# Performance work log

Measured on AMD Instinct MI355X. Metric: run time of the kernel, lower is better.

## Reference

```python
import jax, jax.numpy as jnp
import numpy as np
from jax import lax

E = 300   # word embedding dim (hard-coded embedding_size in DMCNN)
P = 5     # position-feature dim
H = 200   # conv out channels
S = 256   # max_seq_len
L = 34    # num_labels
VOCAB = 21128


def setup_inputs() -> dict:
    key = jax.random.key(0)
    ks = jax.random.split(key, 7)
    B = 8
    return {
        "inputs": jax.random.randint(ks[0], (B, S), 0, VOCAB, dtype=jnp.int64),
        "word_emb": jax.random.normal(ks[1], (VOCAB, E), dtype=jnp.float32) * 0.02,
        "pf_emb": jax.random.normal(ks[2], (S, P), dtype=jnp.float32) * 0.02,
        "conv_W": jax.random.normal(ks[3], (H, E + P, 3), dtype=jnp.float32) * 0.02,
        "conv_b": jax.random.normal(ks[4], (H,), dtype=jnp.float32) * 0.02,
        "fc_W": jax.random.normal(ks[5], (L, 3 * E + 2 * H), dtype=jnp.float32) * 0.02,
        "fc_b": jax.random.normal(ks[6], (L,), dtype=jnp.float32) * 0.02,
    }


def _conv1d(x_ncs, w_oik):
    # x: [N, C, S], w: [O, I, K], stride 1, padding 1 (kernel 3)
    return lax.conv_general_dilated(
        x_ncs, w_oik, window_strides=(1,), padding=[(1, 1)],
        dimension_numbers=("NCH", "OIH", "NCH"))


def reference(inputs, word_emb, pf_emb, conv_W, conv_b, fc_W, fc_b):
    B = inputs.shape[0]
    tok = word_emb[inputs]                       # [B, S, E]

    # Positions i = 1 .. S-2 (the original loop), fully vectorized.
    i_vals = jnp.arange(1, S - 1)                # [S-2]
    j = jnp.arange(S)
    pos_idx = jnp.abs(j[None, :] - i_vals[:, None])   # [S-2, S] == the loop's pos_index
    pf = pf_emb[pos_idx]                         # [S-2, S, P]

    # Conv is linear: split into token part (shared across i) + pf part (per i).
    W_tok, W_pf = conv_W[:, :E, :], conv_W[:, E:, :]
    conv_tok = _conv1d(tok.transpose(0, 2, 1), W_tok) + conv_b[None, :, None]  # [B, H, S]
    conv_pf = _conv1d(pf.transpose(0, 2, 1), W_pf)                             # [S-2, H, S] (batch-independent)

    out = jax.nn.relu(conv_tok[None] + conv_pf[:, None])   # [S-2, B, H, S]

    # Dynamic split max-pool at index i.
    left_mask = (j[None, :] < i_vals[:, None])[:, None, None, :]  # [S-2,1,1,S]
    neg_inf = jnp.array(-jnp.inf, dtype=out.dtype)
    max_left = jnp.where(left_mask, out, neg_inf).max(axis=-1)    # [S-2, B, H]
    max_right = jnp.where(left_mask, neg_inf, out).max(axis=-1)   # [S-2, B, H]
    pool = jnp.concatenate([max_left, max_right], axis=-1)        # [S-2, B, 2H]

    # Lexical-level features: window [i-1, i, i+1] flattened.
    llf = jnp.concatenate([tok[:, 0:S - 2], tok[:, 1:S - 1], tok[:, 2:S]], axis=-1)  # [B, S-2, 3E]

    feat = jnp.concatenate([pool.transpose(1, 0, 2), llf], axis=-1)  # [B, S-2, 2H+3E]
    logits_mid = jnp.einsum("bsf,lf->bsl", feat, fc_W) + fc_b        # [B, S-2, L]

    pad = jnp.zeros((B, 1, L), dtype=logits_mid.dtype).at[:, :, -1].set(1.0)
    return jnp.concatenate([pad, logits_mid, pad], axis=1)          # [B, S, L]
```

## Files before the change

kernel.cpp:

```cpp
#include <hip/hip_runtime.h>

#define E 300
#define P 5
#define H 200
#define S 256
#define L 34
#define B 8
#define NI 254

typedef __attribute__((ext_vector_type(8))) _Float16 half8;
typedef __attribute__((ext_vector_type(2))) _Float16 h2;
typedef __attribute__((ext_vector_type(4))) float f32x4;

#define TOKB_OFF   0
#define TOKB_FL    309632
#define WR3_OFF    309632
#define WR3_FL     96512
#define FCWB_OFF   406144
#define FCWB_FL    32256
#define G_OFF      438400
#define G_FL       51200
#define C0_OFF     489600
#define C0_FL      25400
#define C255_OFF   515000
#define C255_FL    25400
#define CT_OFF     540400
#define CT_FL      204800
#define POOLF_OFF  745200
#define POOLF_FL   425984

__device__ __forceinline__ unsigned short f2h(float f) {
    _Float16 h = (_Float16)f;
    unsigned short u; __builtin_memcpy(&u, &h, 2);
    return u;
}
__device__ __forceinline__ h2 u2h2(unsigned u) {
    h2 h; __builtin_memcpy(&h, &u, 4); return h;
}
__device__ __forceinline__ unsigned h2u(h2 h) {
    unsigned u; __builtin_memcpy(&u, &h, 4); return u;
}
__device__ __forceinline__ h2 hmax2(h2 a, h2 b) {
    return __builtin_elementwise_max(a, b);
}
__device__ __forceinline__ half8 load_h8(const unsigned short* p) {
    half8 r;
    ((ushort4*)&r)[0] = *(const ushort4*)p;
    ((ushort4*)&r)[1] = *(const ushort4*)(p + 4);
    return r;
}

#define GA_BLOCKS 605
#define PREP_BLOCKS 1803

__global__ __launch_bounds__(256) void k_init(const int* __restrict__ ids,
                                              const float* __restrict__ we,
                                              const float* __restrict__ convW,
                                              const float* __restrict__ fcW,
                                              const float* __restrict__ pf,
                                              unsigned short* __restrict__ tokb,
                                              unsigned short* __restrict__ Wr3,
                                              unsigned short* __restrict__ fcWb,
                                              unsigned short* __restrict__ g,
                                              unsigned short* __restrict__ c0,
                                              unsigned short* __restrict__ c255) {
    if (blockIdx.x < GA_BLOCKS) {
        int idx = blockIdx.x * 256 + threadIdx.x;
        const int total = B * 258 * 75;
        if (idx >= total) return;
        int row = idx / 75;
        int col = idx - row * 75;
        int b = row / 258;
        int r = row - b * 258;
        float4 v = make_float4(0.f, 0.f, 0.f, 0.f);
        if (r >= 1 && r <= 256) {
            int id = ids[b * S + (r - 1)];
            v = ((const float4*)we)[(size_t)id * 75 + col];
        }
        ushort4 o;
        o.x = f2h(v.x); o.y = f2h(v.y); o.z = f2h(v.z); o.w = f2h(v.w);
        *(ushort4*)(tokb + (size_t)row * 300 + col * 4) = o;
        return;
    }
    int idx = (blockIdx.x - GA_BLOCKS) * 256 + threadIdx.x;
    if (idx < 193024) {
        int hh = idx / 928, kk = idx - hh * 928;
        float v = 0.f;
        if (hh < H && kk < 900) {
            int r = kk / 300, e = kk - r * 300;
            v = convW[hh * 915 + e * 3 + r];
        }
        Wr3[idx] = f2h(v);
    } else if (idx < 257536) {
        int t = idx - 193024;
        int l = t / 1344, c = t - l * 1344;
        float v = 0.f;
        if (l < L) {
            if (c < 400) v = fcW[l * 1300 + c];
            else if (c >= 416 && c < 1316) v = fcW[l * 1300 + 400 + (c - 416)];
        }
        fcWb[t] = f2h(v);
    } else if (idx < 359936) {
        int t = idx - 257536;
        int t2 = t / H, h = t - t2 * H;
        int d = t2 - 256;
        float a = 0.f;
#pragma unroll
        for (int k = 0; k < 3; k++) {
            int r = d + k - 1; r = (r < 0) ? -r : r; if (r > 255) r = 255;
#pragma unroll
            for (int q = 0; q < P; q++)
                a += convW[h * 915 + (E + q) * 3 + k] * pf[r * P + q];
        }
        g[t] = f2h(a);
    } else if (idx < 410736) {
        int t = idx - 359936;
        int m = t / H, h = t - m * H;
        int i = m + 1;
        float a = 0.f;
#pragma unroll
        for (int q = 0; q < P; q++) {
            a += convW[h * 915 + (E + q) * 3 + 1] * pf[i * P + q];
            a += convW[h * 915 + (E + q) * 3 + 2] * pf[(i - 1) * P + q];
        }
        c0[m * H + h] = f2h(a);
    } else if (idx < 461536) {
        int t = idx - 410736;
        int m = t / H, h = t - m * H;
        int i = m + 1;
        float a = 0.f;
#pragma unroll
        for (int q = 0; q < P; q++) {
            a += convW[h * 915 + (E + q) * 3 + 0] * pf[(254 - i) * P + q];
            a += convW[h * 915 + (E + q) * 3 + 1] * pf[(255 - i) * P + q];
        }
        c255[m * H + h] = f2h(a);
    }
}

__global__ __launch_bounds__(256) void k_conv(const unsigned short* __restrict__ tokb,
                                              const unsigned short* __restrict__ Wr3,
                                              const float* __restrict__ convB,
                                              unsigned short* __restrict__ ct) {
    int n0 = blockIdx.x * 16;
    int mg = blockIdx.y;
    int wave = threadIdx.x >> 6;
    int lane = threadIdx.x & 63;
    int quad = lane >> 4;
    int lr = lane & 15;
    int mtile = mg * 4 + wave;
    int b = mtile >> 4;
    int j0 = (mtile & 15) << 4;

    const unsigned short* pa = tokb + ((size_t)(b * 258 + j0 + lr) * 300 + quad * 8);
    const unsigned short* pb = Wr3 + ((size_t)(n0 + lr) * 928 + quad * 8);

    f32x4 acc0 = {0.f, 0.f, 0.f, 0.f};
    f32x4 acc1 = {0.f, 0.f, 0.f, 0.f};
#pragma unroll
    for (int kk = 0; kk + 1 < 29; kk += 2) {
        half8 a0 = load_h8(pa + kk * 32);
        half8 b0 = load_h8(pb + kk * 32);
        acc0 = __builtin_amdgcn_mfma_f32_16x16x32_f16(a0, b0, acc0, 0, 0, 0);
        half8 a1 = load_h8(pa + kk * 32 + 32);
        half8 b1 = load_h8(pb + kk * 32 + 32);
        acc1 = __builtin_amdgcn_mfma_f32_16x16x32_f16(a1, b1, acc1, 0, 0, 0);
    }
    {
        half8 a0 = load_h8(pa + 28 * 32);
        half8 b0 = load_h8(pb + 28 * 32);
        acc0 = __builtin_amdgcn_mfma_f32_16x16x32_f16(a0, b0, acc0, 0, 0, 0);
    }
    int h = n0 + lr;
    if (h < H) {
        float bias = convB[h];
#pragma unroll
        for (int r = 0; r < 4; r++)
            ct[(size_t)(b * 256 + j0 + quad * 4 + r) * 200 + h] = f2h(acc0[r] + acc1[r] + bias);
    }
}

__global__ __launch_bounds__(512) void k_poolA(const unsigned short* __restrict__ ct,
                                               const unsigned short* __restrict__ g,
                                               const unsigned short* __restrict__ c0,
                                               const unsigned short* __restrict__ c255,
                                               unsigned short* __restrict__ poolf) {
    __shared__ uint2 lds2[8 * 4 * 2 * 50];
    int pg = blockIdx.x;
    int b  = blockIdx.y;
    int tid = threadIdx.x;
    int sub = tid >> 6;
    int lane = tid & 63;
    int p0 = pg * 4 + 1;

    if (lane < 50) {
        int h = lane << 2;
        const unsigned short* ctb = ct + (size_t)b * S * H + h;
        const unsigned short* gb  = g + h;

        h2 z = {(_Float16)0, (_Float16)0};
        h2 aL0a=z, aL0b=z, aL1a=z, aL1b=z, aL2a=z, aL2b=z, aL3a=z, aL3b=z;
        h2 aR0a=z, aR0b=z, aR1a=z, aR1b=z, aR2a=z, aR2b=z, aR3a=z, aR3b=z;

        if (sub == 0) {
            uint2 cu = *(const uint2*)ctb;
            h2 ca = u2h2(cu.x), cb = u2h2(cu.y);
            int m = pg * 4;
            if (m + 0 < NI) { uint2 t = *(const uint2*)(c0 + (m+0) * H + h);
                aL0a = hmax2(aL0a, ca + u2h2(t.x)); aL0b = hmax2(aL0b, cb + u2h2(t.y)); }
            if (m + 1 < NI) { uint2 t = *(const uint2*)(c0 + (m+1) * H + h);
                aL1a = hmax2(aL1a, ca + u2h2(t.x)); aL1b = hmax2(aL1b, cb + u2h2(t.y)); }
            if (m + 2 < NI) { uint2 t = *(const uint2*)(c0 + (m+2) * H + h);
                aL2a = hmax2(aL2a, ca + u2h2(t.x)); aL2b = hmax2(aL2b, cb + u2h2(t.y)); }
            if (m + 3 < NI) { uint2 t = *(const uint2*)(c0 + (m+3) * H + h);
                aL3a = hmax2(aL3a, ca + u2h2(t.x)); aL3b = hmax2(aL3b, cb + u2h2(t.y)); }
        }
        if (sub == 7) {
            uint2 cu = *(const uint2*)(ctb + (size_t)255 * H);
            h2 ca = u2h2(cu.x), cb = u2h2(cu.y);
            int m = pg * 4;
            if (m + 0 < NI) { uint2 t = *(const uint2*)(c255 + (m+0) * H + h);
                aR0a = hmax2(aR0a, ca + u2h2(t.x)); aR0b = hmax2(aR0b, cb + u2h2(t.y)); }
            if (m + 1 < NI) { uint2 t = *(const uint2*)(c255 + (m+1) * H + h);
                aR1a = hmax2(aR1a, ca + u2h2(t.x)); aR1b = hmax2(aR1b, cb + u2h2(t.y)); }
            if (m + 2 < NI) { uint2 t = *(const uint2*)(c255 + (m+2) * H + h);
                aR2a = hmax2(aR2a, ca + u2h2(t.x)); aR2b = hmax2(aR2b, cb + u2h2(t.y)); }
            if (m + 3 < NI) { uint2 t = *(const uint2*)(c255 + (m+3) * H + h);
                aR3a = hmax2(aR3a, ca + u2h2(t.x)); aR3b = hmax2(aR3b, cb + u2h2(t.y)); }
        }

        int js = (sub == 0) ? 1 : sub * 32;
        int je = (sub == 7) ? 254 : sub * 32 + 31;

        uint2 gu;
        gu = *(const uint2*)(gb + (size_t)(js - p0 + 256) * H); h2 gr0a = u2h2(gu.x), gr0b = u2h2(gu.y);
        gu = *(const uint2*)(gb + (size_t)(js - p0 + 255) * H); h2 gr1a = u2h2(gu.x), gr1b = u2h2(gu.y);
        gu = *(const uint2*)(gb + (size_t)(js - p0 + 254) * H); h2 gr2a = u2h2(gu.x), gr2b = u2h2(gu.y);
        gu = *(const uint2*)(gb + (size_t)(js - p0 + 253) * H); h2 gr3a = u2h2(gu.x), gr3b = u2h2(gu.y);

        int eL = (je + 1 < p0) ? (je + 1) : p0;
        int mS = (js > p0) ? js : p0;
        int eM = (je + 1 < p0 + 4) ? (je + 1) : (p0 + 4);
        int rS = (js > p0 + 4) ? js : (p0 + 4);

#pragma unroll 4
        for (int j = js; j < eL; ++j) {
            uint2 cu = *(const uint2*)(ctb + (size_t)j * H);
            h2 ca = u2h2(cu.x), cb = u2h2(cu.y);
            aL0a = hmax2(aL0a, ca + gr0a); aL0b = hmax2(aL0b, cb + gr0b);
            aL1a = hmax2(aL1a, ca + gr1a); aL1b = hmax2(aL1b, cb + gr1b);
            aL2a = hmax2(aL2a, ca + gr2a); aL2b = hmax2(aL2b, cb + gr2b);
            aL3a = hmax2(aL3a, ca + gr3a); aL3b = hmax2(aL3b, cb + gr3b);
            gr3a = gr2a; gr3b = gr2b; gr2a = gr1a; gr2b = gr1b; gr1a = gr0a; gr1b = gr0b;
            uint2 gn = *(const uint2*)(gb + (size_t)(j + 1 - p0 + 256) * H);
            gr0a = u2h2(gn.x); gr0b = u2h2(gn.y);
        }
        for (int j = mS; j < eM; ++j) {
            uint2 cu = *(const uint2*)(ctb + (size_t)j * H);
            h2 ca = u2h2(cu.x), cb = u2h2(cu.y);
            h2 v0a = ca + gr0a, v0b = cb + gr0b;
            h2 v1a = ca + gr1a, v1b = cb + gr1b;
            h2 v2a = ca + gr2a, v2b = cb + gr2b;
            h2 v3a = ca + gr3a, v3b = cb + gr3b;
            if (j < p0)     { aL0a = hmax2(aL0a, v0a); aL0b = hmax2(aL0b, v0b); }
            else            { aR0a = hmax2(aR0a, v0a); aR0b = hmax2(aR0b, v0b); }
            if (j < p0 + 1) { aL1a = hmax2(aL1a, v1a); aL1b = hmax2(aL1b, v1b); }
            else            { aR1a = hmax2(aR1a, v1a); aR1b = hmax2(aR1b, v1b); }
            if (j < p0 + 2) { aL2a = hmax2(aL2a, v2a); aL2b = hmax2(aL2b, v2b); }
            else            { aR2a = hmax2(aR2a, v2a); aR2b = hmax2(aR2b, v2b); }
            if (j < p0 + 3) { aL3a = hmax2(aL3a, v3a); aL3b = hmax2(aL3b, v3b); }
            else            { aR3a = hmax2(aR3a, v3a); aR3b = hmax2(aR3b, v3b); }
            gr3a = gr2a; gr3b = gr2b; gr2a = gr1a; gr2b = gr1b; gr1a = gr0a; gr1b = gr0b;
            uint2 gn = *(const uint2*)(gb + (size_t)(j + 1 - p0 + 256) * H);
            gr0a = u2h2(gn.x); gr0b = u2h2(gn.y);
        }
#pragma unroll 4
        for (int j = rS; j <= je; ++j) {
            uint2 cu = *(const uint2*)(ctb + (size_t)j * H);
            h2 ca = u2h2(cu.x), cb = u2h2(cu.y);
            aR0a = hmax2(aR0a, ca + gr0a); aR0b = hmax2(aR0b, cb + gr0b);
            aR1a = hmax2(aR1a, ca + gr1a); aR1b = hmax2(aR1b, cb + gr1b);
            aR2a = hmax2(aR2a, ca + gr2a); aR2b = hmax2(aR2b, cb + gr2b);
            aR3a = hmax2(aR3a, ca + gr3a); aR3b = hmax2(aR3b, cb + gr3b);
            gr3a = gr2a; gr3b = gr2b; gr2a = gr1a; gr2b = gr1b; gr1a = gr0a; gr1b = gr0b;
            uint2 gn = *(const uint2*)(gb + (size_t)(j + 1 - p0 + 256) * H);
            gr0a = u2h2(gn.x); gr0b = u2h2(gn.y);
        }

        uint2* lp = lds2 + (size_t)sub * 400 + lane;
        lp[0]   = make_uint2(h2u(aL0a), h2u(aL0b)); lp[50]  = make_uint2(h2u(aR0a), h2u(aR0b));
        lp[100] = make_uint2(h2u(aL1a), h2u(aL1b)); lp[150] = make_uint2(h2u(aR1a), h2u(aR1b));
        lp[200] = make_uint2(h2u(aL2a), h2u(aL2b)); lp[250] = make_uint2(h2u(aR2a), h2u(aR2b));
        lp[300] = make_uint2(h2u(aL3a), h2u(aL3b)); lp[350] = make_uint2(h2u(aR3a), h2u(aR3b));
    }
    __syncthreads();

    if (tid < 400) {
        int k = tid / 100;
        int r = tid - k * 100;
        int hf = r / 50;
        int ln = r - hf * 50;
        int slot = (k * 2 + hf) * 50 + ln;
        uint2 v = lds2[slot];
        h2 va = u2h2(v.x), vb = u2h2(v.y);
#pragma unroll
        for (int s2 = 1; s2 < 8; s2++) {
            uint2 w = lds2[s2 * 400 + slot];
            va = hmax2(va, u2h2(w.x));
            vb = hmax2(vb, u2h2(w.y));
        }
        int m = pg * 4 + k;
        if (m < NI)
            *(uint2*)(poolf + (size_t)(b * 256 + m + 1) * 416 + hf * 200 + ln * 4)
                = make_uint2(h2u(va), h2u(vb));
    } else if (tid < 464) {
        int t = tid - 400;
        int k = t >> 4, c = t & 15;
        int m = pg * 4 + k;
        if (m < NI) poolf[(size_t)(b * 256 + m + 1) * 416 + 400 + c] = 0;
    }
}

__global__ __launch_bounds__(256) void k_fc(const unsigned short* __restrict__ poolf,
                                            const unsigned short* __restrict__ tokb,
                                            const unsigned short* __restrict__ fcWb,
                                            const float* __restrict__ fcB,
                                            float* __restrict__ out) {
    int n0 = blockIdx.x * 16;
    int mg = blockIdx.y;
    int wave = threadIdx.x >> 6;
    int lane = threadIdx.x & 63;
    int quad = lane >> 4;
    int lr = lane & 15;
    int mtile = mg * 4 + wave;
    int b = mtile >> 4;
    int s0 = (mtile & 15) << 4;

    const unsigned short* pa0 = poolf + ((size_t)(b * 256 + s0 + lr) * 416 + quad * 8);
    const unsigned short* pa1 = tokb + ((size_t)(b * 258 + s0 + lr) * 300 + quad * 8);
    const unsigned short* pb0 = fcWb + ((size_t)(n0 + lr) * 1344 + quad * 8);
    const unsigned short* pb1 = pb0 + 416;

    f32x4 acc0 = {0.f, 0.f, 0.f, 0.f};
    f32x4 acc1 = {0.f, 0.f, 0.f, 0.f};
    int kk = 0;
#pragma unroll 3
    for (kk = 0; kk + 1 < 13; kk += 2) {
        half8 a0 = load_h8(pa0 + kk * 32);
        half8 b0 = load_h8(pb0 + kk * 32);
        acc0 = __builtin_amdgcn_mfma_f32_16x16x32_f16(a0, b0, acc0, 0, 0, 0);
        half8 a1 = load_h8(pa0 + kk * 32 + 32);
        half8 b1 = load_h8(pb0 + kk * 32 + 32);
        acc1 = __builtin_amdgcn_mfma_f32_16x16x32_f16(a1, b1, acc1, 0, 0, 0);
    }
    {
        half8 a0 = load_h8(pa0 + 12 * 32);
        half8 b0 = load_h8(pb0 + 12 * 32);
        acc0 = __builtin_amdgcn_mfma_f32_16x16x32_f16(a0, b0, acc0, 0, 0, 0);
    }
#pragma unroll 4
    for (kk = 0; kk + 1 < 29; kk += 2) {
        half8 a0 = load_h8(pa1 + kk * 32);
        half8 b0 = load_h8(pb1 + kk * 32);
        acc0 = __builtin_amdgcn_mfma_f32_16x16x32_f16(a0, b0, acc0, 0, 0, 0);
        half8 a1 = load_h8(pa1 + kk * 32 + 32);
        half8 b1 = load_h8(pb1 + kk * 32 + 32);
        acc1 = __builtin_amdgcn_mfma_f32_16x16x32_f16(a1, b1, acc1, 0, 0, 0);
    }
    {
        half8 a0 = load_h8(pa1 + 28 * 32);
        half8 b0 = load_h8(pb1 + 28 * 32);
        acc0 = __builtin_amdgcn_mfma_f32_16x16x32_f16(a0, b0, acc0, 0, 0, 0);
    }

    int l = n0 + lr;
    if (l < L) {
        float bias = fcB[l];
#pragma unroll
        for (int r = 0; r < 4; r++) {
            int s = s0 + quad * 4 + r;
            float val;
            if (s == 0 || s == S - 1) val = (l == L - 1) ? 1.0f : 0.0f;
            else                      val = acc0[r] + acc1[r] + bias;
            out[(size_t)(b * 256 + s) * L + l] = val;
        }
    }
}

extern "C" void kernel_launch(void* const* d_in, const int* in_sizes, int n_in,
                              void* d_out, int out_size, void* d_ws, size_t ws_size,
                              hipStream_t stream) {
    const int*   ids      = (const int*)d_in[0];
    const float* word_emb = (const float*)d_in[1];
    const float* pf_emb   = (const float*)d_in[2];
    const float* conv_W   = (const float*)d_in[3];
    const float* conv_b   = (const float*)d_in[4];
    const float* fc_W     = (const float*)d_in[5];
    const float* fc_b     = (const float*)d_in[6];
    float* out = (float*)d_out;
    float* ws  = (float*)d_ws;

    unsigned short* tokb  = (unsigned short*)(ws + TOKB_OFF);
    unsigned short* Wr3   = (unsigned short*)(ws + WR3_OFF);
    unsigned short* fcWb  = (unsigned short*)(ws + FCWB_OFF);
    unsigned short* g     = (unsigned short*)(ws + G_OFF);
    unsigned short* c0    = (unsigned short*)(ws + C0_OFF);
    unsigned short* c255  = (unsigned short*)(ws + C255_OFF);
    unsigned short* ct    = (unsigned short*)(ws + CT_OFF);
    unsigned short* poolf = (unsigned short*)(ws + POOLF_OFF);

    k_init<<<GA_BLOCKS + PREP_BLOCKS, 256, 0, stream>>>(ids, word_emb, conv_W, fc_W,
                                                        pf_emb, tokb, Wr3, fcWb,
                                                        g, c0, c255);
    k_conv<<<dim3(13, 32), 256, 0, stream>>>(tokb, Wr3, conv_b, ct);
    k_poolA<<<dim3(64, 8), 512, 0, stream>>>(ct, g, c0, c255, poolf);
    k_fc<<<dim3(3, 32), 256, 0, stream>>>(poolf, tokb, fcWb, fc_b, out);
}
```

Baseline: 119.5 us.

## Split K dimension across two wave groups in conv and fc GEMMs

Doubles the block size of k_conv and k_fc to 512 threads and has the second group of four waves compute the other half of the K reduction. The partial sums are combined through shared memory after a block barrier. This shortens each wave's serial MFMA/load chain and exposes more memory-level parallelism for these small, latency-bound GEMMs. The cost is an LDS round trip, a __syncthreads, and half the waves sitting idle during the epilogue.

```diff
diff --git a/kernel.cpp b/kernel.cpp
--- a/kernel.cpp
+++ b/kernel.cpp
@@ -138,17 +138,21 @@
     }
 }
 
-__global__ __launch_bounds__(256) void k_conv(const unsigned short* __restrict__ tokb,
+__global__ __launch_bounds__(512) void k_conv(const unsigned short* __restrict__ tokb,
                                               const unsigned short* __restrict__ Wr3,
                                               const float* __restrict__ convB,
                                               unsigned short* __restrict__ ct) {
+    __shared__ float4 cld[4 * 64];
     int n0 = blockIdx.x * 16;
     int mg = blockIdx.y;
-    int wave = threadIdx.x >> 6;
-    int lane = threadIdx.x & 63;
+    int tid = threadIdx.x;
+    int wave = tid >> 6;
+    int lane = tid & 63;
+    int mt = wave & 3;
+    int kh = wave >> 2;
     int quad = lane >> 4;
     int lr = lane & 15;
-    int mtile = mg * 4 + wave;
+    int mtile = mg * 4 + mt;
     int b = mtile >> 4;
     int j0 = (mtile & 15) << 4;
 
@@ -157,26 +161,47 @@
 
     f32x4 acc0 = {0.f, 0.f, 0.f, 0.f};
     f32x4 acc1 = {0.f, 0.f, 0.f, 0.f};
-#pragma unroll
-    for (int kk = 0; kk + 1 < 29; kk += 2) {
-        half8 a0 = load_h8(pa + kk * 32);
-        half8 b0 = load_h8(pb + kk * 32);
-        acc0 = __builtin_amdgcn_mfma_f32_16x16x32_f16(a0, b0, acc0, 0, 0, 0);
-        half8 a1 = load_h8(pa + kk * 32 + 32);
-        half8 b1 = load_h8(pb + kk * 32 + 32);
-        acc1 = __builtin_amdgcn_mfma_f32_16x16x32_f16(a1, b1, acc1, 0, 0, 0);
-    }
-    {
-        half8 a0 = load_h8(pa + 28 * 32);
-        half8 b0 = load_h8(pb + 28 * 32);
-        acc0 = __builtin_amdgcn_mfma_f32_16x16x32_f16(a0, b0, acc0, 0, 0, 0);
-    }
-    int h = n0 + lr;
-    if (h < H) {
-        float bias = convB[h];
-#pragma unroll
-        for (int r = 0; r < 4; r++)
-            ct[(size_t)(b * 256 + j0 + quad * 4 + r) * 200 + h] = f2h(acc0[r] + acc1[r] + bias);
+    if (kh == 0) {
+#pragma unroll
+        for (int kk = 0; kk < 14; kk += 2) {
+            half8 a0 = load_h8(pa + kk * 32);
+            half8 b0 = load_h8(pb + kk * 32);
+            acc0 = __builtin_amdgcn_mfma_f32_16x16x32_f16(a0, b0, acc0, 0, 0, 0);
+            half8 a1 = load_h8(pa + kk * 32 + 32);
+            half8 b1 = load_h8(pb + kk * 32 + 32);
+            acc1 = __builtin_amdgcn_mfma_f32_16x16x32_f16(a1, b1, acc1, 0, 0, 0);
+        }
+    } else {
+#pragma unroll
+        for (int kk = 14; kk + 1 < 29; kk += 2) {
+            half8 a0 = load_h8(pa + kk * 32);
+            half8 b0 = load_h8(pb + kk * 32);
+            acc0 = __builtin_amdgcn_mfma_f32_16x16x32_f16(a0, b0, acc0, 0, 0, 0);
+            half8 a1 = load_h8(pa + kk * 32 + 32);
+            half8 b1 = load_h8(pb + kk * 32 + 32);
+            acc1 = __builtin_amdgcn_mfma_f32_16x16x32_f16(a1, b1, acc1, 0, 0, 0);
+        }
+        {
+            half8 a0 = load_h8(pa + 28 * 32);
+            half8 b0 = load_h8(pb + 28 * 32);
+            acc0 = __builtin_amdgcn_mfma_f32_16x16x32_f16(a0, b0, acc0, 0, 0, 0);
+        }
+    }
+    f32x4 accw = acc0 + acc1;
+    if (kh == 1) {
+        cld[mt * 64 + lane] = make_float4(accw[0], accw[1], accw[2], accw[3]);
+    }
+    __syncthreads();
+    if (kh == 0) {
+        float4 p = cld[mt * 64 + lane];
+        int h = n0 + lr;
+        if (h < H) {
+            float bias = convB[h];
+            ct[(size_t)(b * 256 + j0 + quad * 4 + 0) * 200 + h] = f2h(accw[0] + p.x + bias);
+            ct[(size_t)(b * 256 + j0 + quad * 4 + 1) * 200 + h] = f2h(accw[1] + p.y + bias);
+            ct[(size_t)(b * 256 + j0 + quad * 4 + 2) * 200 + h] = f2h(accw[2] + p.z + bias);
+            ct[(size_t)(b * 256 + j0 + quad * 4 + 3) * 200 + h] = f2h(accw[3] + p.w + bias);
+        }
     }
 }
 
@@ -321,68 +346,91 @@
     }
 }
 
-__global__ __launch_bounds__(256) void k_fc(const unsigned short* __restrict__ poolf,
+__global__ __launch_bounds__(512) void k_fc(const unsigned short* __restrict__ poolf,
                                             const unsigned short* __restrict__ tokb,
                                             const unsigned short* __restrict__ fcWb,
                                             const float* __restrict__ fcB,
                                             float* __restrict__ out) {
+    __shared__ float4 cld[4 * 64];
     int n0 = blockIdx.x * 16;
     int mg = blockIdx.y;
-    int wave = threadIdx.x >> 6;
-    int lane = threadIdx.x & 63;
+    int tid = threadIdx.x;
+    int wave = tid >> 6;
+    int lane = tid & 63;
+    int mt = wave & 3;
+    int kp = wave >> 2;
     int quad = lane >> 4;
     int lr = lane & 15;
-    int mtile = mg * 4 + wave;
+    int mtile = mg * 4 + mt;
     int b = mtile >> 4;
     int s0 = (mtile & 15) << 4;
 
-    const unsigned short* pa0 = poolf + ((size_t)(b * 256 + s0 + lr) * 416 + quad * 8);
     const unsigned short* pa1 = tokb + ((size_t)(b * 258 + s0 + lr) * 300 + quad * 8);
-    const unsigned short* pb0 = fcWb + ((size_t)(n0 + lr) * 1344 + quad * 8);
-    const unsigned short* pb1 = pb0 + 416;
+    const unsigned short* pb1 = fcWb + ((size_t)(n0 + lr) * 1344 + 416 + quad * 8);
 
     f32x4 acc0 = {0.f, 0.f, 0.f, 0.f};
     f32x4 acc1 = {0.f, 0.f, 0.f, 0.f};
-    int kk = 0;
-#pragma unroll 3
-    for (kk = 0; kk + 1 < 13; kk += 2) {
-        half8 a0 = load_h8(pa0 + kk * 32);
-        half8 b0 = load_h8(pb0 + kk * 32);
-        acc0 = __builtin_amdgcn_mfma_f32_16x16x32_f16(a0, b0, acc0, 0, 0, 0);
-        half8 a1 = load_h8(pa0 + kk * 32 + 32);
-        half8 b1 = load_h8(pb0 + kk * 32 + 32);
-        acc1 = __builtin_amdgcn_mfma_f32_16x16x32_f16(a1, b1, acc1, 0, 0, 0);
-    }
-    {
-        half8 a0 = load_h8(pa0 + 12 * 32);
-        half8 b0 = load_h8(pb0 + 12 * 32);
-        acc0 = __builtin_amdgcn_mfma_f32_16x16x32_f16(a0, b0, acc0, 0, 0, 0);
-    }
-#pragma unroll 4
-    for (kk = 0; kk + 1 < 29; kk += 2) {
-        half8 a0 = load_h8(pa1 + kk * 32);
-        half8 b0 = load_h8(pb1 + kk * 32);
-        acc0 = __builtin_amdgcn_mfma_f32_16x16x32_f16(a0, b0, acc0, 0, 0, 0);
-        half8 a1 = load_h8(pa1 + kk * 32 + 32);
-        half8 b1 = load_h8(pb1 + kk * 32 + 32);
-        acc1 = __builtin_amdgcn_mfma_f32_16x16x32_f16(a1, b1, acc1, 0, 0, 0);
-    }
-    {
-        half8 a0 = load_h8(pa1 + 28 * 32);
-        half8 b0 = load_h8(pb1 + 28 * 32);
-        acc0 = __builtin_amdgcn_mfma_f32_16x16x32_f16(a0, b0, acc0, 0, 0, 0);
-    }
-
-    int l = n0 + lr;
-    if (l < L) {
-        float bias = fcB[l];
-#pragma unroll
-        for (int r = 0; r < 4; r++) {
-            int s = s0 + quad * 4 + r;
-            float val;
-            if (s == 0 || s == S - 1) val = (l == L - 1) ? 1.0f : 0.0f;
-            else                      val = acc0[r] + acc1[r] + bias;
-            out[(size_t)(b * 256 + s) * L + l] = val;
+    if (kp == 0) {
+        const unsigned short* pa0 = poolf + ((size_t)(b * 256 + s0 + lr) * 416 + quad * 8);
+        const unsigned short* pb0 = fcWb + ((size_t)(n0 + lr) * 1344 + quad * 8);
+#pragma unroll
+        for (int kk = 0; kk + 1 < 13; kk += 2) {
+            half8 a0 = load_h8(pa0 + kk * 32);
+            half8 b0 = load_h8(pb0 + kk * 32);
+            acc0 = __builtin_amdgcn_mfma_f32_16x16x32_f16(a0, b0, acc0, 0, 0, 0);
+            half8 a1 = load_h8(pa0 + kk * 32 + 32);
+            half8 b1 = load_h8(pb0 + kk * 32 + 32);
+            acc1 = __builtin_amdgcn_mfma_f32_16x16x32_f16(a1, b1, acc1, 0, 0, 0);
+        }
+        {
+            half8 a0 = load_h8(pa0 + 12 * 32);
+            half8 b0 = load_h8(pb0 + 12 * 32);
+            acc0 = __builtin_amdgcn_mfma_f32_16x16x32_f16(a0, b0, acc0, 0, 0, 0);
+        }
+#pragma unroll
+        for (int kk = 0; kk < 8; kk += 2) {
+            half8 a0 = load_h8(pa1 + kk * 32);
+            half8 b0 = load_h8(pb1 + kk * 32);
+            acc0 = __builtin_amdgcn_mfma_f32_16x16x32_f16(a0, b0, acc0, 0, 0, 0);
+            half8 a1 = load_h8(pa1 + kk * 32 + 32);
+            half8 b1 = load_h8(pb1 + kk * 32 + 32);
+            acc1 = __builtin_amdgcn_mfma_f32_16x16x32_f16(a1, b1, acc1, 0, 0, 0);
+        }
+    } else {
+#pragma unroll
+        for (int kk = 8; kk + 1 < 29; kk += 2) {
+            half8 a0 = load_h8(pa1 + kk * 32);
+            half8 b0 = load_h8(pb1 + kk * 32);
+            acc0 = __builtin_amdgcn_mfma_f32_16x16x32_f16(a0, b0, acc0, 0, 0, 0);
+            half8 a1 = load_h8(pa1 + kk * 32 + 32);
+            half8 b1 = load_h8(pb1 + kk * 32 + 32);
+            acc1 = __builtin_amdgcn_mfma_f32_16x16x32_f16(a1, b1, acc1, 0, 0, 0);
+        }
+        {
+            half8 a0 = load_h8(pa1 + 28 * 32);
+            half8 b0 = load_h8(pb1 + 28 * 32);
+            acc0 = __builtin_amdgcn_mfma_f32_16x16x32_f16(a0, b0, acc0, 0, 0, 0);
+        }
+    }
+    f32x4 accw = acc0 + acc1;
+    if (kp == 1) {
+        cld[mt * 64 + lane] = make_float4(accw[0], accw[1], accw[2], accw[3]);
+    }
+    __syncthreads();
+    if (kp == 0) {
+        float4 p = cld[mt * 64 + lane];
+        float r4[4] = {accw[0] + p.x, accw[1] + p.y, accw[2] + p.z, accw[3] + p.w};
+        int l = n0 + lr;
+        if (l < L) {
+            float bias = fcB[l];
+#pragma unroll
+            for (int r = 0; r < 4; r++) {
+                int s = s0 + quad * 4 + r;
+                float val;
+                if (s == 0 || s == S - 1) val = (l == L - 1) ? 1.0f : 0.0f;
+                else                      val = r4[r] + bias;
+                out[(size_t)(b * 256 + s) * L + l] = val;
+            }
         }
     }
 }
@@ -412,7 +460,7 @@
     k_init<<<GA_BLOCKS + PREP_BLOCKS, 256, 0, stream>>>(ids, word_emb, conv_W, fc_W,
                                                         pf_emb, tokb, Wr3, fcWb,
                                                         g, c0, c255);
-    k_conv<<<dim3(13, 32), 256, 0, stream>>>(tokb, Wr3, conv_b, ct);
+    k_conv<<<dim3(13, 32), 512, 0, stream>>>(tokb, Wr3, conv_b, ct);
     k_poolA<<<dim3(64, 8), 512, 0, stream>>>(ct, g, c0, c255, poolf);
-    k_fc<<<dim3(3, 32), 256, 0, stream>>>(poolf, tokb, fcWb, fc_b, out);
-}
+    k_fc<<<dim3(3, 32), 512, 0, stream>>>(poolf, tokb, fcWb, fc_b, out);
+}
```

New measurement: 116.9 us. -2.2%, faster.
